# Kernel tuning notes

Hardware: AMD Instinct MI355X
Metric: run time of the kernel (lower is better)

## Reference

```python
import jax, jax.numpy as jnp
import numpy as np

N_HEADS = 16


def setup_inputs() -> dict:
    key = jax.random.key(0)
    k1, k2, k3 = jax.random.split(key, 3)
    B, S, D = 2, 2048, 1024
    x = jax.random.normal(k1, (B, S, D), dtype=jnp.float32)
    w_qkv = jax.random.normal(k2, (D, 3 * D), dtype=jnp.float32) * 0.02
    b_qkv = jnp.zeros((3 * D,), dtype=jnp.float32)
    w_proj = jax.random.normal(k3, (D, D), dtype=jnp.float32) * 0.02
    b_proj = jnp.zeros((D,), dtype=jnp.float32)
    return {"x": x, "w_qkv": w_qkv, "b_qkv": b_qkv, "w_proj": w_proj, "b_proj": b_proj}


def reference(x, w_qkv, b_qkv, w_proj, b_proj):
    # Faithful to CausalAttention.flash_atttention: the blockwise online-softmax
    # loop computes exactly softmax(Q K^T / sqrt(hd) + causal_mask) V (no dropout).
    B, S, D = x.shape
    H = N_HEADS
    hd = D // H
    scale = 1.0 / jnp.sqrt(jnp.asarray(hd, dtype=x.dtype))

    qkv = x @ w_qkv + b_qkv                       # [B, S, 3D]
    q, k, v = jnp.split(qkv, 3, axis=-1)
    q = q.reshape(B, S, H, hd).transpose(0, 2, 1, 3)  # [B, H, S, hd]
    k = k.reshape(B, S, H, hd).transpose(0, 2, 1, 3)
    v = v.reshape(B, S, H, hd).transpose(0, 2, 1, 3)

    scores = jnp.einsum('bhqd,bhkd->bhqk', q, k) * scale  # [B, H, S, S]
    causal = jnp.tril(jnp.ones((S, S), dtype=bool))
    scores = jnp.where(causal, scores, -jnp.inf)
    attn = jax.nn.softmax(scores, axis=-1)
    out = jnp.einsum('bhqk,bhkd->bhqd', attn, v)  # [B, H, S, hd]
    out = out.transpose(0, 2, 1, 3).reshape(B, S, D)
    return out @ w_proj + b_proj
```

## Files before the change

### kernel.cpp

```cpp
#include <hip/hip_runtime.h>
#include <hip/hip_bf16.h>

typedef unsigned short u16;
typedef __attribute__((ext_vector_type(8))) short short8;
typedef __attribute__((ext_vector_type(4))) float floatx4;
typedef __attribute__((ext_vector_type(16))) float floatx16;

__device__ __forceinline__ u16 f2bf(float f) {
  union { float f; unsigned u; } v; v.f = f;
  unsigned r = v.u + 0x7fffu + ((v.u >> 16) & 1u);
  return (u16)(r >> 16);
}

__device__ __forceinline__ floatx4 mfma16(short8 a, short8 b, floatx4 c) {
  return __builtin_amdgcn_mfma_f32_16x16x32_bf16(a, b, c, 0, 0, 0);
}
__device__ __forceinline__ floatx16 mfma32(short8 a, short8 b, floatx16 c) {
  return __builtin_amdgcn_mfma_f32_32x32x16_bf16(a, b, c, 0, 0, 0);
}

#define AS1 __attribute__((address_space(1)))
#define AS3 __attribute__((address_space(3)))
__device__ __forceinline__ void gload_lds16(const u16* g, u16* l) {
  __builtin_amdgcn_global_load_lds((const AS1 void*)g, (AS3 void*)l, 16, 0, 0);
}

__device__ __forceinline__ unsigned pack2(float a, float b) {
  union { __hip_bfloat162 h; unsigned u; } x;
  x.h = __hip_bfloat162(__float2bfloat16(a), __float2bfloat16(b));
  return x.u;
}

__device__ __forceinline__ float fexp2(float x) {
#if __has_builtin(__builtin_amdgcn_exp2f)
  return __builtin_amdgcn_exp2f(x);
#else
  return exp2f(x);
#endif
}

#define WAIT_VM(N) asm volatile("s_waitcnt vmcnt(" #N ")" ::: "memory")
#define BARRIER()                      \
  do {                                 \
    __builtin_amdgcn_s_barrier();      \
    asm volatile("" ::: "memory");     \
  } while (0)

#define QSCALE 0.18033688f

__global__ void __launch_bounds__(256) f32_to_bf16_vec(
    const float* __restrict__ in, u16* __restrict__ out) {
  const int i = blockIdx.x * 256 + threadIdx.x;
  const float4* p = (const float4*)in + (size_t)i * 2;
  float4 a = p[0], b = p[1];
  short8 o;
  o[0] = (short)f2bf(a.x); o[1] = (short)f2bf(a.y);
  o[2] = (short)f2bf(a.z); o[3] = (short)f2bf(a.w);
  o[4] = (short)f2bf(b.x); o[5] = (short)f2bf(b.y);
  o[6] = (short)f2bf(b.z); o[7] = (short)f2bf(b.w);
  *(short8*)(out + (size_t)i * 8) = o;
}

__global__ void __launch_bounds__(256) transpose_f32_to_bf16(
    const float* __restrict__ in, u16* __restrict__ out, int R, int C) {
  __shared__ float tile[64][65];
  const int c0 = blockIdx.x * 64, r0 = blockIdx.y * 64;
  const int t = threadIdx.x;
  const int rr = t >> 2, cc = (t & 3) * 16;
  const float* src = in + (size_t)(r0 + rr) * C + (c0 + cc);
  float4 v0 = *(const float4*)(src);
  float4 v1 = *(const float4*)(src + 4);
  float4 v2 = *(const float4*)(src + 8);
  float4 v3 = *(const float4*)(src + 12);
  tile[rr][cc + 0] = v0.x;  tile[rr][cc + 1] = v0.y;
  tile[rr][cc + 2] = v0.z;  tile[rr][cc + 3] = v0.w;
  tile[rr][cc + 4] = v1.x;  tile[rr][cc + 5] = v1.y;
  tile[rr][cc + 6] = v1.z;  tile[rr][cc + 7] = v1.w;
  tile[rr][cc + 8] = v2.x;  tile[rr][cc + 9] = v2.y;
  tile[rr][cc + 10] = v2.z; tile[rr][cc + 11] = v2.w;
  tile[rr][cc + 12] = v3.x; tile[rr][cc + 13] = v3.y;
  tile[rr][cc + 14] = v3.z; tile[rr][cc + 15] = v3.w;
  __syncthreads();
  short8 w0, w1;
#pragma unroll
  for (int i = 0; i < 8; ++i) {
    w0[i] = (short)f2bf(tile[cc + i][rr]);
    w1[i] = (short)f2bf(tile[cc + 8 + i][rr]);
  }
  u16* dst = out + (size_t)(c0 + rr) * R + (r0 + cc);
  *(short8*)dst = w0;
  *(short8*)(dst + 8) = w1;
}

__global__ void __launch_bounds__(256) gemm_qkv(
    const u16* __restrict__ A, const u16* __restrict__ Bt,
    const float* __restrict__ bias, u16* __restrict__ O0,
    u16* __restrict__ O1, u16* __restrict__ O2, int N, int K) {
  __shared__ u16 As[2][4096];
  __shared__ u16 Bs[2][4096];
  const int t = threadIdx.x, w = t >> 6, l = t & 63;
  const int lo = l & 15, g = l >> 4;
  const int wr = w >> 1, wc = w & 1;
  const int m0 = blockIdx.y * 128, n0 = blockIdx.x * 128;
  const int srow = l >> 2;
  const int schunk = (l & 3) ^ ((l >> 4) & 3);
  const u16* ApS = A + (size_t)(m0 + w * 32 + srow) * K + schunk * 8;
  const u16* BpS = Bt + (size_t)(n0 + w * 32 + srow) * K + schunk * 8;

  floatx4 acc[4][4] = {};
  const int NT = K >> 5;

#define STAGE_G(buf, kt_)                                                    \
  do {                                                                       \
    const size_t k0_ = (size_t)(kt_) * 32;                                   \
    _Pragma("unroll") for (int i = 0; i < 2; ++i)                            \
        gload_lds16(ApS + (size_t)i * 16 * K + k0_,                          \
                    &As[buf][(w * 2 + i) * 512]);                            \
    _Pragma("unroll") for (int i = 0; i < 2; ++i)                            \
        gload_lds16(BpS + (size_t)i * 16 * K + k0_,                          \
                    &Bs[buf][(w * 2 + i) * 512]);                            \
  } while (0)

#define COMPUTE_G(cur)                                                       \
  do {                                                                       \
    short8 af[4], bff[4];                                                    \
    _Pragma("unroll") for (int m = 0; m < 4; ++m) {                          \
      const int row = wr * 64 + m * 16 + lo;                                 \
      const int sl = g ^ ((lo >> 2) & 3);                                    \
      af[m] = *(const short8*)(&As[cur][row * 32 + sl * 8]);                 \
    }                                                                        \
    _Pragma("unroll") for (int n = 0; n < 4; ++n) {                          \
      const int row = wc * 64 + n * 16 + lo;                                 \
      const int sl = g ^ ((lo >> 2) & 3);                                    \
      bff[n] = *(const short8*)(&Bs[cur][row * 32 + sl * 8]);                \
    }                                                                        \
    __builtin_amdgcn_s_setprio(1);                                           \
    _Pragma("unroll") for (int m = 0; m < 4; ++m)                            \
        _Pragma("unroll") for (int n = 0; n < 4; ++n) acc[m][n] =            \
            mfma16(af[m], bff[n], acc[m][n]);                                \
    __builtin_amdgcn_s_setprio(0);                                           \
  } while (0)

  STAGE_G(0, 0);
  int cur = 0;
  for (int kt = 0; kt < NT - 1; ++kt) {
    STAGE_G(cur ^ 1, kt + 1);
    WAIT_VM(4);
    BARRIER();
    COMPUTE_G(cur);
    BARRIER();
    cur ^= 1;
  }
  WAIT_VM(0);
  BARRIER();
  COMPUTE_G(cur);
#undef STAGE_G
#undef COMPUTE_G

#pragma unroll
  for (int m = 0; m < 4; ++m) {
    const int row_base = m0 + wr * 64 + m * 16 + g * 4;
#pragma unroll
    for (int n = 0; n < 4; ++n) {
      const int col = n0 + wc * 64 + n * 16 + lo;
      const float bv = bias[col];
#pragma unroll
      for (int j = 0; j < 4; ++j) {
        const int r = row_base + j;
        const float v = acc[m][n][j] + bv;
        const int b = r >> 11, s = r & 2047;
        int c = col;
        if (c < 1024) {
          const int hh = c >> 6, d = c & 63;
          O0[(((size_t)(b * 16 + hh)) * 2048 + s) * 64 + d] = f2bf(v * QSCALE);
        } else if (c < 2048) {
          c -= 1024;
          const int hh = c >> 6, d = c & 63;
          O1[(((size_t)(b * 16 + hh)) * 2048 + s) * 64 + d] = f2bf(v);
        } else {
          c -= 2048;
          const int hh = c >> 6, d = c & 63;
          O2[(((size_t)(b * 16 + hh)) * 64 + d) * 2048 + s] = f2bf(v);
        }
      }
    }
  }
}

__global__ void __launch_bounds__(256, 2) gemm_proj(
    const u16* __restrict__ A, const u16* __restrict__ Bt,
    const float* __restrict__ bias, float* __restrict__ Of, int N, int K) {
  __shared__ u16 As[2][8192];
  __shared__ u16 Bs[2][8192];
  const int t = threadIdx.x, w = t >> 6, l = t & 63;
  const int lo = l & 15, g = l >> 4;
  const int wr = w >> 1, wc = w & 1;
  const int m0 = blockIdx.y * 128, n0 = blockIdx.x * 128;
  const int srow = l >> 3;
  const int schunk = (l & 7) ^ srow;
  const u16* ApS = A + (size_t)(m0 + w * 32 + srow) * K + schunk * 8;
  const u16* BpS = Bt + (size_t)(n0 + w * 32 + srow) * K + schunk * 8;

  floatx4 acc[4][4] = {};
  const int NT = K >> 6;

#define STAGE_P(buf, kt_)                                                    \
  do {                                                                       \
    const size_t k0_ = (size_t)(kt_) * 64;                                   \
    _Pragma("unroll") for (int i = 0; i < 4; ++i)                            \
        gload_lds16(ApS + (size_t)i * 8 * K + k0_,                           \
                    &As[buf][(w * 4 + i) * 512]);                            \
    _Pragma("unroll") for (int i = 0; i < 4; ++i)                            \
        gload_lds16(BpS + (size_t)i * 8 * K + k0_,                           \
                    &Bs[buf][(w * 4 + i) * 512]);                            \
  } while (0)

#define COMPUTE_P(cur)                                                       \
  do {                                                                       \
    short8 af[2][4], bff[2][4];                                              \
    _Pragma("unroll") for (int kk = 0; kk < 2; ++kk)                         \
        _Pragma("unroll") for (int m = 0; m < 4; ++m) {                      \
      const int row = wr * 64 + m * 16 + lo;                                 \
      const int sl = (kk * 4 + g) ^ (row & 7);                               \
      af[kk][m] = *(const short8*)(&As[cur][row * 64 + sl * 8]);             \
    }                                                                        \
    _Pragma("unroll") for (int kk = 0; kk < 2; ++kk)                         \
        _Pragma("unroll") for (int n = 0; n < 4; ++n) {                      \
      const int row = wc * 64 + n * 16 + lo;                                 \
      const int sl = (kk * 4 + g) ^ (row & 7);                               \
      bff[kk][n] = *(const short8*)(&Bs[cur][row * 64 + sl * 8]);            \
    }                                                                        \
    __builtin_amdgcn_s_setprio(1);                                           \
    _Pragma("unroll") for (int kk = 0; kk < 2; ++kk)                         \
        _Pragma("unroll") for (int m = 0; m < 4; ++m)                        \
            _Pragma("unroll") for (int n = 0; n < 4; ++n) acc[m][n] =        \
                mfma16(af[kk][m], bff[kk][n], acc[m][n]);                    \
    __builtin_amdgcn_s_setprio(0);                                           \
  } while (0)

  STAGE_P(0, 0);
  int cur = 0;
  for (int kt = 0; kt < NT - 1; ++kt) {
    STAGE_P(cur ^ 1, kt + 1);
    WAIT_VM(8);
    BARRIER();
    COMPUTE_P(cur);
    BARRIER();
    cur ^= 1;
  }
  WAIT_VM(0);
  BARRIER();
  COMPUTE_P(cur);
#undef STAGE_P
#undef COMPUTE_P

#pragma unroll
  for (int m = 0; m < 4; ++m) {
    const int row_base = m0 + wr * 64 + m * 16 + g * 4;
#pragma unroll
    for (int n = 0; n < 4; ++n) {
      const int col = n0 + wc * 64 + n * 16 + lo;
      const float bv = bias[col];
#pragma unroll
      for (int j = 0; j < 4; ++j) {
        const int r = row_base + j;
        __builtin_nontemporal_store(acc[m][n][j] + bv,
                                    &Of[(size_t)r * N + col]);
      }
    }
  }
}

__global__ void __launch_bounds__(256, 2) attn_kernel(
    const u16* __restrict__ Q, const u16* __restrict__ K,
    const u16* __restrict__ Vt, u16* __restrict__ O) {
  const int S = 2048;
  __shared__ u16 smem[2][16384];
  const int t = threadIdx.x, w = t >> 6, l = t & 63;
  const int lo = l & 31, h = l >> 5;
  const int wg = blockIdx.x;
  const int bh = (wg & 7) * 4 + ((wg >> 3) & 3);
  const int qidx = wg >> 5;
  const int qb = (qidx < 8) ? qidx : 23 - qidx;
  const int q0w = qb * 128 + w * 32;
  const int qabs = q0w + lo;
  const u16* Qb = Q + (size_t)bh * S * 64;
  const u16* Kb = K + (size_t)bh * S * 64;
  const u16* Vb = Vt + (size_t)bh * 64 * S;

  short8 qf[4];
#pragma unroll
  for (int ks = 0; ks < 4; ++ks)
    qf[ks] = *(const short8*)(Qb + (size_t)(q0w + lo) * 64 + ks * 16 + h * 8);

  floatx16 o0 = {}, o1 = {};
  float ll = 0.f;

  auto STAGE = [&](int buf, int tile) {
    const int kv0 = tile * 128;
#pragma unroll
    for (int i = 0; i < 4; ++i) {
      const int idx = i * 256 + t;
      const int rw = idx >> 3;
      const int cg = (idx & 7) ^ (rw & 7);
      gload_lds16(Kb + (size_t)(kv0 + rw) * 64 + cg * 8,
                  &smem[buf][(i * 256 + w * 64) * 8]);
    }
#pragma unroll
    for (int i = 0; i < 4; ++i) {
      const int idx = i * 256 + t;
      const int rw = idx >> 4;
      const int cg = (idx & 15) ^ (rw & 15);
      gload_lds16(Vb + (size_t)rw * S + kv0 + cg * 8,
                  &smem[buf][8192 + (i * 256 + w * 64) * 8]);
    }
  };

  auto COMPUTE = [&](int cur, int kv0) {
    floatx16 st[4] = {};
    __builtin_amdgcn_s_setprio(1);
#pragma unroll
    for (int ks = 0; ks < 4; ++ks)
#pragma unroll
      for (int nt = 0; nt < 4; ++nt) {
        const int row = nt * 32 + lo;
        short8 kf = *(const short8*)(
            &smem[cur][row * 64 + (((ks * 2 + h) ^ (row & 7)) * 8)]);
        st[nt] = mfma32(kf, qf[ks], st[nt]);
      }
    __builtin_amdgcn_s_setprio(0);
    const bool diag = (kv0 + 127 > q0w);
    float p[4][16];
#pragma unroll
    for (int nt = 0; nt < 4; ++nt)
#pragma unroll
      for (int rr = 0; rr < 16; ++rr) {
        float v = st[nt][rr];
        if (diag) {
          const int kvr = kv0 + nt * 32 + (rr & 3) + 8 * (rr >> 2) + 4 * h;
          if (kvr > qabs) v = -1e30f;
        }
        const float e = fexp2(v);
        p[nt][rr] = e;
        ll += e;
      }
    __builtin_amdgcn_s_setprio(1);
#pragma unroll
    for (int s = 0; s < 8; ++s) {
      const int nt = s >> 1, rb = (s & 1) * 8;
      const unsigned wA = pack2(p[nt][rb + 0], p[nt][rb + 1]);
      const unsigned wB = pack2(p[nt][rb + 2], p[nt][rb + 3]);
      const unsigned wC = pack2(p[nt][rb + 4], p[nt][rb + 5]);
      const unsigned wD = pack2(p[nt][rb + 6], p[nt][rb + 7]);
      union { unsigned u[4]; short8 s8; } bf;
#if __has_builtin(__builtin_amdgcn_permlane32_swap)
      auto r02 = __builtin_amdgcn_permlane32_swap((int)wA, (int)wC, false, false);
      auto r13 = __builtin_amdgcn_permlane32_swap((int)wB, (int)wD, false, false);
      bf.u[0] = (unsigned)r02[0];
      bf.u[1] = (unsigned)r13[0];
      bf.u[2] = (unsigned)r02[1];
      bf.u[3] = (unsigned)r13[1];
#else
      const unsigned sA = (unsigned)__shfl_xor((int)wA, 32);
      const unsigned sB = (unsigned)__shfl_xor((int)wB, 32);
      const unsigned sC = (unsigned)__shfl_xor((int)wC, 32);
      const unsigned sD = (unsigned)__shfl_xor((int)wD, 32);
      bf.u[0] = h ? sC : wA;
      bf.u[1] = h ? sD : wB;
      bf.u[2] = h ? wC : sA;
      bf.u[3] = h ? wD : sB;
#endif
      {
        const int d = lo;
        short8 vf = *(const short8*)(
            &smem[cur][8192 + d * 128 + (((s * 2 + h) ^ (d & 15)) * 8)]);
        o0 = mfma32(vf, bf.s8, o0);
      }
      {
        const int d = 32 + lo;
        short8 vf = *(const short8*)(
            &smem[cur][8192 + d * 128 + (((s * 2 + h) ^ (d & 15)) * 8)]);
        o1 = mfma32(vf, bf.s8, o1);
      }
    }
    __builtin_amdgcn_s_setprio(0);
  };

  const int T = qb + 1;
  STAGE(0, 0);
  int cur = 0;
  for (int tt = 0; tt < T - 1; ++tt) {
    STAGE(cur ^ 1, tt + 1);
    WAIT_VM(8);
    BARRIER();
    COMPUTE(cur, tt * 128);
    BARRIER();
    cur ^= 1;
  }
  WAIT_VM(0);
  BARRIER();
  COMPUTE(cur, (T - 1) * 128);
  __syncthreads();

  ll += __shfl_xor(ll, 32);
  const float rl = 1.0f / ll;
  u16* ep = &smem[0][w * 2048];
#pragma unroll
  for (int rr = 0; rr < 16; ++rr) {
    const int d0 = (rr & 3) + 8 * (rr >> 2) + 4 * h;
    ep[lo * 64 + (d0 ^ ((lo & 7) << 3))] = f2bf(o0[rr] * rl);
    const int d1 = d0 + 32;
    ep[lo * 64 + (d1 ^ ((lo & 7) << 3))] = f2bf(o1[rr] * rl);
  }
  __builtin_amdgcn_s_barrier();
  const int hh = bh & 15, b = bh >> 4;
  u16* Ob = O + ((size_t)(b * 2048 + q0w)) * 1024 + hh * 64;
#pragma unroll
  for (int pp = 0; pp < 4; ++pp) {
    const int idx = pp * 64 + l;
    const int row = idx >> 3, c = idx & 7;
    short8 v = *(const short8*)(&ep[row * 64 + ((c * 8) ^ ((row & 7) << 3))]);
    *(short8*)(Ob + (size_t)row * 1024 + c * 8) = v;
  }
}

extern "C" void kernel_launch(void* const* d_in, const int* in_sizes, int n_in,
                              void* d_out, int out_size, void* d_ws,
                              size_t ws_size, hipStream_t stream) {
  const float* x = (const float*)d_in[0];
  const float* w_qkv = (const float*)d_in[1];
  const float* b_qkv = (const float*)d_in[2];
  const float* w_proj = (const float*)d_in[3];
  const float* b_proj = (const float*)d_in[4];
  float* out = (float*)d_out;

  char* ws = (char*)d_ws;
  u16* Xb = (u16*)(ws);
  u16* WqkvT = (u16*)(ws + 8388608);
  u16* WprojT = (u16*)(ws + 14680064);
  u16* Qw = (u16*)(ws + 16777216);
  u16* Kw = (u16*)(ws + 25165824);
  u16* Vtw = (u16*)(ws + 33554432);
  u16* AttnO = Xb;

  f32_to_bf16_vec<<<2048, 256, 0, stream>>>(x, Xb);
  transpose_f32_to_bf16<<<dim3(48, 16), 256, 0, stream>>>(w_qkv, WqkvT, 1024,
                                                          3072);
  transpose_f32_to_bf16<<<dim3(16, 16), 256, 0, stream>>>(w_proj, WprojT, 1024,
                                                          1024);
  gemm_qkv<<<dim3(24, 32), 256, 0, stream>>>(Xb, WqkvT, b_qkv, Qw, Kw, Vtw,
                                             3072, 1024);
  attn_kernel<<<512, 256, 0, stream>>>(Qw, Kw, Vtw, AttnO);
  gemm_proj<<<dim3(8, 32), 256, 0, stream>>>(AttnO, WprojT, b_proj, out, 1024,
                                             1024);
}
```

Measured before the change: 127.4 us.

## Halve K/V and proj tiles, skip fully-masked causal tiles per wave

The attention kernel now stages 64-row K/V tiles instead of 128, halving shared memory per block. Each wave skips compute on tiles lying entirely above its causal diagonal, which removes wasted masked MFMA and exp work on the diagonal block. The projection GEMM drops its K-tile from 64 to 32, also halving LDS, and both kernels lose the min-blocks launch bound. In exchange there are twice as many barriers and pipeline iterations, and the V layout/swizzle changes, so the tile-loading indices must stay consistent.

New measurement: 138.4 us. +8.6%, slower.

```diff
diff --git a/kernel.cpp b/kernel.cpp
--- a/kernel.cpp
+++ b/kernel.cpp
@@ -187,54 +187,51 @@
   }
 }
 
-__global__ void __launch_bounds__(256, 2) gemm_proj(
+__global__ void __launch_bounds__(256) gemm_proj(
     const u16* __restrict__ A, const u16* __restrict__ Bt,
     const float* __restrict__ bias, float* __restrict__ Of, int N, int K) {
-  __shared__ u16 As[2][8192];
-  __shared__ u16 Bs[2][8192];
+  __shared__ u16 As[2][4096];
+  __shared__ u16 Bs[2][4096];
   const int t = threadIdx.x, w = t >> 6, l = t & 63;
   const int lo = l & 15, g = l >> 4;
   const int wr = w >> 1, wc = w & 1;
   const int m0 = blockIdx.y * 128, n0 = blockIdx.x * 128;
-  const int srow = l >> 3;
-  const int schunk = (l & 7) ^ srow;
+  const int srow = l >> 2;
+  const int schunk = (l & 3) ^ ((l >> 4) & 3);
   const u16* ApS = A + (size_t)(m0 + w * 32 + srow) * K + schunk * 8;
   const u16* BpS = Bt + (size_t)(n0 + w * 32 + srow) * K + schunk * 8;
 
   floatx4 acc[4][4] = {};
-  const int NT = K >> 6;
+  const int NT = K >> 5;
 
 #define STAGE_P(buf, kt_)                                                    \
   do {                                                                       \
-    const size_t k0_ = (size_t)(kt_) * 64;                                   \
-    _Pragma("unroll") for (int i = 0; i < 4; ++i)                            \
-        gload_lds16(ApS + (size_t)i * 8 * K + k0_,                           \
-                    &As[buf][(w * 4 + i) * 512]);                            \
-    _Pragma("unroll") for (int i = 0; i < 4; ++i)                            \
-        gload_lds16(BpS + (size_t)i * 8 * K + k0_,                           \
-                    &Bs[buf][(w * 4 + i) * 512]);                            \
+    const size_t k0_ = (size_t)(kt_) * 32;                                   \
+    _Pragma("unroll") for (int i = 0; i < 2; ++i)                            \
+        gload_lds16(ApS + (size_t)i * 16 * K + k0_,                          \
+                    &As[buf][(w * 2 + i) * 512]);                            \
+    _Pragma("unroll") for (int i = 0; i < 2; ++i)                            \
+        gload_lds16(BpS + (size_t)i * 16 * K + k0_,                          \
+                    &Bs[buf][(w * 2 + i) * 512]);                            \
   } while (0)
 
 #define COMPUTE_P(cur)                                                       \
   do {                                                                       \
-    short8 af[2][4], bff[2][4];                                              \
-    _Pragma("unroll") for (int kk = 0; kk < 2; ++kk)                         \
-        _Pragma("unroll") for (int m = 0; m < 4; ++m) {                      \
+    short8 af[4], bff[4];                                                    \
+    _Pragma("unroll") for (int m = 0; m < 4; ++m) {                          \
       const int row = wr * 64 + m * 16 + lo;                                 \
-      const int sl = (kk * 4 + g) ^ (row & 7);                               \
-      af[kk][m] = *(const short8*)(&As[cur][row * 64 + sl * 8]);             \
+      const int sl = g ^ ((lo >> 2) & 3);                                    \
+      af[m] = *(const short8*)(&As[cur][row * 32 + sl * 8]);                 \
     }                                                                        \
-    _Pragma("unroll") for (int kk = 0; kk < 2; ++kk)                         \
-        _Pragma("unroll") for (int n = 0; n < 4; ++n) {                      \
+    _Pragma("unroll") for (int n = 0; n < 4; ++n) {                          \
       const int row = wc * 64 + n * 16 + lo;                                 \
-      const int sl = (kk * 4 + g) ^ (row & 7);                               \
-      bff[kk][n] = *(const short8*)(&Bs[cur][row * 64 + sl * 8]);            \
+      const int sl = g ^ ((lo >> 2) & 3);                                    \
+      bff[n] = *(const short8*)(&Bs[cur][row * 32 + sl * 8]);                \
     }                                                                        \
     __builtin_amdgcn_s_setprio(1);                                           \
-    _Pragma("unroll") for (int kk = 0; kk < 2; ++kk)                         \
-        _Pragma("unroll") for (int m = 0; m < 4; ++m)                        \
-            _Pragma("unroll") for (int n = 0; n < 4; ++n) acc[m][n] =        \
-                mfma16(af[kk][m], bff[kk][n], acc[m][n]);                    \
+    _Pragma("unroll") for (int m = 0; m < 4; ++m)                            \
+        _Pragma("unroll") for (int n = 0; n < 4; ++n) acc[m][n] =            \
+            mfma16(af[m], bff[n], acc[m][n]);                                \
     __builtin_amdgcn_s_setprio(0);                                           \
   } while (0)
 
@@ -242,7 +239,7 @@
   int cur = 0;
   for (int kt = 0; kt < NT - 1; ++kt) {
     STAGE_P(cur ^ 1, kt + 1);
-    WAIT_VM(8);
+    WAIT_VM(4);
     BARRIER();
     COMPUTE_P(cur);
     BARRIER();
@@ -271,11 +268,11 @@
   }
 }
 
-__global__ void __launch_bounds__(256, 2) attn_kernel(
+__global__ void __launch_bounds__(256) attn_kernel(
     const u16* __restrict__ Q, const u16* __restrict__ K,
     const u16* __restrict__ Vt, u16* __restrict__ O) {
   const int S = 2048;
-  __shared__ u16 smem[2][16384];
+  __shared__ u16 smem[2][8192];
   const int t = threadIdx.x, w = t >> 6, l = t & 63;
   const int lo = l & 31, h = l >> 5;
   const int wg = blockIdx.x;
@@ -283,6 +280,7 @@
   const int qidx = wg >> 5;
   const int qb = (qidx < 8) ? qidx : 23 - qidx;
   const int q0w = qb * 128 + w * 32;
+  const int qmax = q0w + 31;
   const int qabs = q0w + lo;
   const u16* Qb = Q + (size_t)bh * S * 64;
   const u16* Kb = K + (size_t)bh * S * 64;
@@ -297,61 +295,59 @@
   float ll = 0.f;
 
   auto STAGE = [&](int buf, int tile) {
-    const int kv0 = tile * 128;
-#pragma unroll
-    for (int i = 0; i < 4; ++i) {
+    const int kv0 = tile * 64;
+#pragma unroll
+    for (int i = 0; i < 2; ++i) {
       const int idx = i * 256 + t;
       const int rw = idx >> 3;
       const int cg = (idx & 7) ^ (rw & 7);
       gload_lds16(Kb + (size_t)(kv0 + rw) * 64 + cg * 8,
-                  &smem[buf][(i * 256 + w * 64) * 8]);
-    }
-#pragma unroll
-    for (int i = 0; i < 4; ++i) {
-      const int idx = i * 256 + t;
-      const int rw = idx >> 4;
-      const int cg = (idx & 15) ^ (rw & 15);
+                  &smem[buf][i * 2048 + w * 512]);
       gload_lds16(Vb + (size_t)rw * S + kv0 + cg * 8,
-                  &smem[buf][8192 + (i * 256 + w * 64) * 8]);
+                  &smem[buf][4096 + i * 2048 + w * 512]);
     }
   };
 
   auto COMPUTE = [&](int cur, int kv0) {
-    floatx16 st[4] = {};
+    floatx16 st0 = {}, st1 = {};
     __builtin_amdgcn_s_setprio(1);
 #pragma unroll
-    for (int ks = 0; ks < 4; ++ks)
-#pragma unroll
-      for (int nt = 0; nt < 4; ++nt) {
-        const int row = nt * 32 + lo;
-        short8 kf = *(const short8*)(
-            &smem[cur][row * 64 + (((ks * 2 + h) ^ (row & 7)) * 8)]);
-        st[nt] = mfma32(kf, qf[ks], st[nt]);
+    for (int ks = 0; ks < 4; ++ks) {
+      const int r0 = lo;
+      short8 kf0 = *(const short8*)(
+          &smem[cur][r0 * 64 + ((ks * 16 + h * 8) ^ ((r0 & 7) << 3))]);
+      st0 = mfma32(kf0, qf[ks], st0);
+      const int r1 = 32 + lo;
+      short8 kf1 = *(const short8*)(
+          &smem[cur][r1 * 64 + ((ks * 16 + h * 8) ^ ((r1 & 7) << 3))]);
+      st1 = mfma32(kf1, qf[ks], st1);
+    }
+    __builtin_amdgcn_s_setprio(0);
+    const bool diag = (kv0 + 63 > q0w);
+    float p[2][16];
+#pragma unroll
+    for (int rr = 0; rr < 16; ++rr) {
+      float v0 = st0[rr];
+      float v1 = st1[rr];
+      if (diag) {
+        const int kvr = kv0 + (rr & 3) + 8 * (rr >> 2) + 4 * h;
+        if (kvr > qabs) v0 = -1e30f;
+        if (kvr + 32 > qabs) v1 = -1e30f;
       }
-    __builtin_amdgcn_s_setprio(0);
-    const bool diag = (kv0 + 127 > q0w);
-    float p[4][16];
-#pragma unroll
-    for (int nt = 0; nt < 4; ++nt)
-#pragma unroll
-      for (int rr = 0; rr < 16; ++rr) {
-        float v = st[nt][rr];
-        if (diag) {
-          const int kvr = kv0 + nt * 32 + (rr & 3) + 8 * (rr >> 2) + 4 * h;
-          if (kvr > qabs) v = -1e30f;
-        }
-        const float e = fexp2(v);
-        p[nt][rr] = e;
-        ll += e;
-      }
+      const float e0 = fexp2(v0);
+      const float e1 = fexp2(v1);
+      p[0][rr] = e0;
+      p[1][rr] = e1;
+      ll += e0 + e1;
+    }
     __builtin_amdgcn_s_setprio(1);
 #pragma unroll
-    for (int s = 0; s < 8; ++s) {
-      const int nt = s >> 1, rb = (s & 1) * 8;
-      const unsigned wA = pack2(p[nt][rb + 0], p[nt][rb + 1]);
-      const unsigned wB = pack2(p[nt][rb + 2], p[nt][rb + 3]);
-      const unsigned wC = pack2(p[nt][rb + 4], p[nt][rb + 5]);
-      const unsigned wD = pack2(p[nt][rb + 6], p[nt][rb + 7]);
+    for (int s = 0; s < 4; ++s) {
+      const int ts = s >> 1, rb = (s & 1) * 8;
+      const unsigned wA = pack2(p[ts][rb + 0], p[ts][rb + 1]);
+      const unsigned wB = pack2(p[ts][rb + 2], p[ts][rb + 3]);
+      const unsigned wC = pack2(p[ts][rb + 4], p[ts][rb + 5]);
+      const unsigned wD = pack2(p[ts][rb + 6], p[ts][rb + 7]);
       union { unsigned u[4]; short8 s8; } bf;
 #if __has_builtin(__builtin_amdgcn_permlane32_swap)
       auto r02 = __builtin_amdgcn_permlane32_swap((int)wA, (int)wC, false, false);
@@ -371,35 +367,39 @@
       bf.u[3] = h ? wD : sB;
 #endif
       {
-        const int d = lo;
+        const int r0 = lo;
         short8 vf = *(const short8*)(
-            &smem[cur][8192 + d * 128 + (((s * 2 + h) ^ (d & 15)) * 8)]);
+            &smem[cur][4096 + r0 * 64 + ((s * 16 + h * 8) ^ ((r0 & 7) << 3))]);
         o0 = mfma32(vf, bf.s8, o0);
       }
       {
-        const int d = 32 + lo;
+        const int r1 = 32 + lo;
         short8 vf = *(const short8*)(
-            &smem[cur][8192 + d * 128 + (((s * 2 + h) ^ (d & 15)) * 8)]);
+            &smem[cur][4096 + r1 * 64 + ((s * 16 + h * 8) ^ ((r1 & 7) << 3))]);
         o1 = mfma32(vf, bf.s8, o1);
       }
     }
     __builtin_amdgcn_s_setprio(0);
   };
 
-  const int T = qb + 1;
+  const int T = 2 * (qb + 1);
   STAGE(0, 0);
   int cur = 0;
   for (int tt = 0; tt < T - 1; ++tt) {
     STAGE(cur ^ 1, tt + 1);
-    WAIT_VM(8);
-    BARRIER();
-    COMPUTE(cur, tt * 128);
+    WAIT_VM(4);
+    BARRIER();
+    const int kv0 = tt * 64;
+    if (kv0 <= qmax) COMPUTE(cur, kv0);
     BARRIER();
     cur ^= 1;
   }
   WAIT_VM(0);
   BARRIER();
-  COMPUTE(cur, (T - 1) * 128);
+  {
+    const int kv0 = (T - 1) * 64;
+    if (kv0 <= qmax) COMPUTE(cur, kv0);
+  }
   __syncthreads();
 
   ll += __shfl_xor(ll, 32);
```
